# Kernel tuning notes

Measured on AMD Instinct MI355X. Metric: run time of the kernel, lower is better.

Reference implementation:

```python
import jax, jax.numpy as jnp
import numpy as np

N_NODES = 16   # number of per-node submodules in the DAG (topological order)
D = 2048       # per-node feature width (d_model)
B = 4096       # batch size of the in_graph tensor


def setup_inputs() -> dict:
    key = jax.random.key(0)
    kx, kw, kb = jax.random.split(key, 3)
    x = jax.random.normal(kx, (B, D), dtype=jnp.float32)
    # Per-node dense weights, scaled ~1/sqrt(D) so tanh stays in its linear-ish range
    W = jax.random.normal(kw, (N_NODES, D, D), dtype=jnp.float32) / np.float32(np.sqrt(D))
    b = jax.random.normal(kb, (N_NODES, D), dtype=jnp.float32) * np.float32(0.01)
    return {"x": x, "W": W, "b": b}


def reference(x, W, b):
    # Faithful DAG executor: iterate nodes in topological order; the address
    # book maps node i -> predecessor outputs {i-1, i-2} (node 0 reads x).
    # Each node module computes y = tanh(sum(inputs) @ W_i + b_i).
    # Loop is over the fixed structural node set (not a data dimension).
    outs = []
    for i in range(N_NODES):
        if i == 0:
            inp = x
        elif i == 1:
            inp = outs[0]
        else:
            inp = outs[i - 1] + outs[i - 2]  # address-book fan-in (sum of predecessors)
        y = jnp.tanh(inp @ W[i] + b[i])  # [B, D]
        outs.append(y)
    # _eval_forward returns the single terminal output of the DAG
    return outs[-1]
```

## Files before the change

### kernel.cpp

```cpp
#include <hip/hip_runtime.h>
#include <cstdint>
#include <cstddef>

#define NN 16
#define DD 2048
#define BB 4096

#define TM 256
#define TN 128
#define BK 64
#define BUFH (TM * BK + TN * BK)

typedef _Float16 half8 __attribute__((ext_vector_type(8)));
typedef _Float16 half4 __attribute__((ext_vector_type(4)));
typedef float f32x4 __attribute__((ext_vector_type(4)));

__device__ __forceinline__ float fast_tanh(float x) {
  float ax = __builtin_fabsf(x);
  float e = __expf(-2.0f * ax);
  float t = (1.0f - e) / (1.0f + e);
  return x < 0.0f ? -t : t;
}

__global__ __launch_bounds__(256) void wconv_kernel(const float* __restrict__ W,
                                                    _Float16* __restrict__ Wh) {
  __shared__ _Float16 tile[64][80];
  const int i = blockIdx.z;
  const int k0 = blockIdx.y * 64;
  const int n0 = blockIdx.x * 64;
  const float* Wi = W + (size_t)i * DD * DD;
  _Float16* Whi = Wh + (size_t)i * DD * DD;
  const int t = threadIdx.x;
  const int cr = t >> 4;
  const int cc = (t & 15) * 4;
#pragma unroll
  for (int p = 0; p < 4; ++p) {
    int r = p * 16 + cr;
    float4 v = *(const float4*)(Wi + (size_t)(k0 + r) * DD + n0 + cc);
    tile[cc + 0][r] = (_Float16)v.x;
    tile[cc + 1][r] = (_Float16)v.y;
    tile[cc + 2][r] = (_Float16)v.z;
    tile[cc + 3][r] = (_Float16)v.w;
  }
  __syncthreads();
  const int wr = t >> 3;
  const int wc = (t & 7) * 8;
#pragma unroll
  for (int p = 0; p < 2; ++p) {
    int n = p * 32 + wr;
    half8 v = *(const half8*)&tile[n][wc];
    *(half8*)(Whi + (size_t)(n0 + n) * DD + k0 + wc) = v;
  }
}

__global__ __launch_bounds__(256) void xconv_kernel(const float* __restrict__ x,
                                                    _Float16* __restrict__ s0) {
  size_t idx = (size_t)(blockIdx.x * 256 + threadIdx.x) * 4;
  float4 v = *(const float4*)(x + idx);
  half4 o;
  o.x = (_Float16)v.x; o.y = (_Float16)v.y; o.z = (_Float16)v.z; o.w = (_Float16)v.w;
  *(half4*)(s0 + idx) = o;
}

__global__ __launch_bounds__(512, 2) void node_gemm(
    const _Float16* __restrict__ S,
    const _Float16* __restrict__ Wt,
    const float* __restrict__ bias,
    _Float16* __restrict__ Y,
    const _Float16* __restrict__ Yprev,
    _Float16* __restrict__ Snext,
    float* __restrict__ Ofinal)
{
  __shared__ _Float16 smem[3 * BUFH];

  const int t = threadIdx.x;
  const int lane = t & 63;
  const int wave = t >> 6;
  const int bid = blockIdx.x;
  const int swz = (bid & 7) * 32 + (bid >> 3);
  const int n0 = (swz >> 4) * TN;
  const int m0 = (swz & 15) * TM;
  const int wm = (wave >> 1) * 64;
  const int wn = (wave & 1) * 64;
  const int lrow = lane & 15;
  const int lq = lane >> 4;

  f32x4 acc[4][4];
#pragma unroll
  for (int i = 0; i < 4; ++i)
#pragma unroll
    for (int j = 0; j < 4; ++j) acc[i][j] = (f32x4)0.0f;

  const int srow = t >> 3;
  const int ska = ((t & 7) ^ (srow & 7)) * 8;
  const _Float16* ag = S + (size_t)(m0 + srow) * DD + ska;
  const _Float16* bg = Wt + (size_t)(n0 + srow) * DD + ska;

  auto stage = [&](int buf, int k0) {
    const _Float16* a = ag + k0;
    const _Float16* b = bg + k0;
    _Float16* al = smem + buf * BUFH + t * 8;
    _Float16* bl = smem + buf * BUFH + TM * BK + t * 8;
#pragma unroll
    for (int r = 0; r < 4; ++r)
      __builtin_amdgcn_global_load_lds(
          (const __attribute__((address_space(1))) void*)(a + (size_t)(r * 64) * DD),
          (__attribute__((address_space(3))) void*)(al + r * 4096), 16, 0, 0);
#pragma unroll
    for (int r = 0; r < 2; ++r)
      __builtin_amdgcn_global_load_lds(
          (const __attribute__((address_space(1))) void*)(b + (size_t)(r * 64) * DD),
          (__attribute__((address_space(3))) void*)(bl + r * 4096), 16, 0, 0);
  };

  stage(0, 0);
  stage(1, BK);
  asm volatile("s_waitcnt vmcnt(6)" ::: "memory");
  asm volatile("s_barrier" ::: "memory");

  int cur = 0, nxt = 2;
  for (int i = 0; i < DD / BK; ++i) {
    if (i <= DD / BK - 3) stage(nxt, (i + 2) * BK);
    const _Float16* Ap = smem + cur * BUFH;
    const _Float16* Bp = smem + cur * BUFH + TM * BK;
#pragma unroll
    for (int ks = 0; ks < BK; ks += 32) {
      const int cx = (((ks >> 3) + lq) ^ (lrow & 7)) * 8;
      half8 a[4], b[4];
#pragma unroll
      for (int mt = 0; mt < 4; ++mt)
        a[mt] = *(const half8*)(Ap + (wm + mt * 16 + lrow) * BK + cx);
#pragma unroll
      for (int nt = 0; nt < 4; ++nt)
        b[nt] = *(const half8*)(Bp + (wn + nt * 16 + lrow) * BK + cx);
      __builtin_amdgcn_s_setprio(1);
#pragma unroll
      for (int mt = 0; mt < 4; ++mt)
#pragma unroll
        for (int nt = 0; nt < 4; ++nt)
          acc[mt][nt] =
              __builtin_amdgcn_mfma_f32_16x16x32_f16(a[mt], b[nt], acc[mt][nt], 0, 0, 0);
      __builtin_amdgcn_s_setprio(0);
    }
    if (i < DD / BK - 2) {
      asm volatile("s_waitcnt vmcnt(6)" ::: "memory");
      asm volatile("s_barrier" ::: "memory");
    } else if (i == DD / BK - 2) {
      asm volatile("s_waitcnt vmcnt(0)" ::: "memory");
      asm volatile("s_barrier" ::: "memory");
    }
    cur = (cur == 2) ? 0 : cur + 1;
    nxt = (nxt == 2) ? 0 : nxt + 1;
  }

  __syncthreads();
  _Float16* CT = smem;
  float bv[4];
#pragma unroll
  for (int nt = 0; nt < 4; ++nt) bv[nt] = bias[n0 + wn + nt * 16 + lrow];
#pragma unroll
  for (int mt = 0; mt < 4; ++mt)
#pragma unroll
    for (int nt = 0; nt < 4; ++nt)
#pragma unroll
      for (int r = 0; r < 4; ++r) {
        int row = wm + mt * 16 + lq * 4 + r;
        int col = wn + nt * 16 + lrow;
        CT[row * TN + col] = (_Float16)fast_tanh(acc[mt][nt][r] + bv[nt]);
      }
  __syncthreads();

#pragma unroll
  for (int pp = 0; pp < 8; ++pp) {
    int idx = pp * 4096 + t * 8;
    int row = idx >> 7;
    int col = idx & 127;
    size_t off = (size_t)(m0 + row) * DD + n0 + col;
    half8 y = *(const half8*)&CT[idx];
    if (Ofinal) {
      float4 f0 = {(float)y[0], (float)y[1], (float)y[2], (float)y[3]};
      float4 f1 = {(float)y[4], (float)y[5], (float)y[6], (float)y[7]};
      *(float4*)(Ofinal + off) = f0;
      *(float4*)(Ofinal + off + 4) = f1;
    } else {
      *(half8*)(Y + off) = y;
      half8 s = y;
      if (Yprev) s = s + *(const half8*)(Yprev + off);
      *(half8*)(Snext + off) = s;
    }
  }
}

extern "C" void kernel_launch(void* const* d_in, const int* in_sizes, int n_in,
                              void* d_out, int out_size, void* d_ws, size_t ws_size,
                              hipStream_t stream) {
  const float* x = (const float*)d_in[0];
  const float* W = (const float*)d_in[1];
  const float* b = (const float*)d_in[2];
  float* out = (float*)d_out;
  char* ws = (char*)d_ws;

  _Float16* Wh = (_Float16*)ws;
  size_t wbytes = (size_t)NN * DD * DD * sizeof(_Float16);
  _Float16* S0 = (_Float16*)(ws + wbytes);
  _Float16* S1 = S0 + (size_t)BB * DD;
  _Float16* Y0 = S1 + (size_t)BB * DD;
  _Float16* Y1 = Y0 + (size_t)BB * DD;

  wconv_kernel<<<dim3(DD / 64, DD / 64, NN), dim3(256), 0, stream>>>(W, Wh);
  xconv_kernel<<<dim3((BB * DD) / 1024), dim3(256), 0, stream>>>(x, S0);

  _Float16* Sb[2] = {S0, S1};
  _Float16* Yb[2] = {Y0, Y1};
  dim3 ggrid((BB / TM) * (DD / TN));
  for (int i = 0; i < NN; ++i) {
    const _Float16* Sin = Sb[i & 1];
    _Float16* Sout = Sb[(i + 1) & 1];
    _Float16* Yout = Yb[i & 1];
    const _Float16* Yp = (i >= 1) ? Yb[(i + 1) & 1] : nullptr;
    const bool last = (i == NN - 1);
    node_gemm<<<ggrid, dim3(512), 0, stream>>>(Sin, Wh + (size_t)i * DD * DD,
                                               b + (size_t)i * DD, Yout, Yp, Sout,
                                               last ? out : nullptr);
  }
  (void)in_sizes; (void)n_in; (void)out_size; (void)ws_size;
}
```

Before: 1.134 ms.

## Interleave prefetch issue with MFMA phases and remap tiles to XCD-local blocks

Splits each K-iteration into four phases. Each phase loads a subset of the A/B fragments from LDS, issues part of the next stage's global-to-LDS prefetch, hits a barrier, and runs eight MFMAs. This spreads memory issue across the compute instead of bursting it at loop start. The tile mapping is also changed so each XCD gets a contiguous 4x8 block of output tiles, which should improve L2 reuse of S rows and W columns. The extra barriers per iteration add synchronisation overhead and may stall waves.

```diff
diff --git a/kernel.cpp b/kernel.cpp
--- a/kernel.cpp
+++ b/kernel.cpp
@@ -77,9 +77,10 @@
   const int lane = t & 63;
   const int wave = t >> 6;
   const int bid = blockIdx.x;
-  const int swz = (bid & 7) * 32 + (bid >> 3);
-  const int n0 = (swz >> 4) * TN;
-  const int m0 = (swz & 15) * TM;
+  const int xcd = bid & 7;
+  const int loc = bid >> 3;
+  const int m0 = ((xcd & 3) * 4 + (loc & 3)) * TM;
+  const int n0 = ((xcd >> 2) * 8 + (loc >> 2)) * TN;
   const int wm = (wave >> 1) * 64;
   const int wn = (wave & 1) * 64;
   const int lrow = lane & 15;
@@ -96,16 +97,18 @@
   const _Float16* ag = S + (size_t)(m0 + srow) * DD + ska;
   const _Float16* bg = Wt + (size_t)(n0 + srow) * DD + ska;
 
-  auto stage = [&](int buf, int k0) {
+  auto stageA2 = [&](int buf, int k0, int r0) {
     const _Float16* a = ag + k0;
+    _Float16* al = smem + buf * BUFH + t * 8;
+#pragma unroll
+    for (int r = 0; r < 2; ++r)
+      __builtin_amdgcn_global_load_lds(
+          (const __attribute__((address_space(1))) void*)(a + (size_t)((r0 + r) * 64) * DD),
+          (__attribute__((address_space(3))) void*)(al + (r0 + r) * 4096), 16, 0, 0);
+  };
+  auto stageB2 = [&](int buf, int k0) {
     const _Float16* b = bg + k0;
-    _Float16* al = smem + buf * BUFH + t * 8;
     _Float16* bl = smem + buf * BUFH + TM * BK + t * 8;
-#pragma unroll
-    for (int r = 0; r < 4; ++r)
-      __builtin_amdgcn_global_load_lds(
-          (const __attribute__((address_space(1))) void*)(a + (size_t)(r * 64) * DD),
-          (__attribute__((address_space(3))) void*)(al + r * 4096), 16, 0, 0);
 #pragma unroll
     for (int r = 0; r < 2; ++r)
       __builtin_amdgcn_global_load_lds(
@@ -113,42 +116,79 @@
           (__attribute__((address_space(3))) void*)(bl + r * 4096), 16, 0, 0);
   };
 
-  stage(0, 0);
-  stage(1, BK);
+  stageA2(0, 0, 0); stageA2(0, 0, 2); stageB2(0, 0);
+  stageA2(1, BK, 0); stageA2(1, BK, 2); stageB2(1, BK);
   asm volatile("s_waitcnt vmcnt(6)" ::: "memory");
   asm volatile("s_barrier" ::: "memory");
 
   int cur = 0, nxt = 2;
   for (int i = 0; i < DD / BK; ++i) {
-    if (i <= DD / BK - 3) stage(nxt, (i + 2) * BK);
     const _Float16* Ap = smem + cur * BUFH;
     const _Float16* Bp = smem + cur * BUFH + TM * BK;
-#pragma unroll
-    for (int ks = 0; ks < BK; ks += 32) {
-      const int cx = (((ks >> 3) + lq) ^ (lrow & 7)) * 8;
-      half8 a[4], b[4];
-#pragma unroll
-      for (int mt = 0; mt < 4; ++mt)
-        a[mt] = *(const half8*)(Ap + (wm + mt * 16 + lrow) * BK + cx);
-#pragma unroll
-      for (int nt = 0; nt < 4; ++nt)
-        b[nt] = *(const half8*)(Bp + (wn + nt * 16 + lrow) * BK + cx);
-      __builtin_amdgcn_s_setprio(1);
-#pragma unroll
-      for (int mt = 0; mt < 4; ++mt)
-#pragma unroll
-        for (int nt = 0; nt < 4; ++nt)
-          acc[mt][nt] =
-              __builtin_amdgcn_mfma_f32_16x16x32_f16(a[mt], b[nt], acc[mt][nt], 0, 0, 0);
-      __builtin_amdgcn_s_setprio(0);
-    }
+    const bool pf = (i <= DD / BK - 3);
+    const int pk = (i + 2) * BK;
+    const int cx0 = ((0 + lq) ^ (lrow & 7)) * 8;
+    const int cx1 = ((4 + lq) ^ (lrow & 7)) * 8;
+    half8 a[4], b[4];
+
+#pragma unroll
+    for (int mt = 0; mt < 4; ++mt)
+      a[mt] = *(const half8*)(Ap + (wm + mt * 16 + lrow) * BK + cx0);
+    b[0] = *(const half8*)(Bp + (wn + 0 + lrow) * BK + cx0);
+    b[1] = *(const half8*)(Bp + (wn + 16 + lrow) * BK + cx0);
+    if (pf) stageA2(nxt, pk, 0);
+    asm volatile("s_barrier" ::: "memory");
+    __builtin_amdgcn_s_setprio(1);
+#pragma unroll
+    for (int mt = 0; mt < 4; ++mt) {
+      acc[mt][0] = __builtin_amdgcn_mfma_f32_16x16x32_f16(a[mt], b[0], acc[mt][0], 0, 0, 0);
+      acc[mt][1] = __builtin_amdgcn_mfma_f32_16x16x32_f16(a[mt], b[1], acc[mt][1], 0, 0, 0);
+    }
+    __builtin_amdgcn_s_setprio(0);
+
+    b[2] = *(const half8*)(Bp + (wn + 32 + lrow) * BK + cx0);
+    b[3] = *(const half8*)(Bp + (wn + 48 + lrow) * BK + cx0);
+    if (pf) stageA2(nxt, pk, 2);
+    asm volatile("s_barrier" ::: "memory");
+    __builtin_amdgcn_s_setprio(1);
+#pragma unroll
+    for (int mt = 0; mt < 4; ++mt) {
+      acc[mt][2] = __builtin_amdgcn_mfma_f32_16x16x32_f16(a[mt], b[2], acc[mt][2], 0, 0, 0);
+      acc[mt][3] = __builtin_amdgcn_mfma_f32_16x16x32_f16(a[mt], b[3], acc[mt][3], 0, 0, 0);
+    }
+    __builtin_amdgcn_s_setprio(0);
+
+#pragma unroll
+    for (int mt = 0; mt < 4; ++mt)
+      a[mt] = *(const half8*)(Ap + (wm + mt * 16 + lrow) * BK + cx1);
+    b[0] = *(const half8*)(Bp + (wn + 0 + lrow) * BK + cx1);
+    b[1] = *(const half8*)(Bp + (wn + 16 + lrow) * BK + cx1);
+    if (pf) stageB2(nxt, pk);
+    asm volatile("s_barrier" ::: "memory");
+    __builtin_amdgcn_s_setprio(1);
+#pragma unroll
+    for (int mt = 0; mt < 4; ++mt) {
+      acc[mt][0] = __builtin_amdgcn_mfma_f32_16x16x32_f16(a[mt], b[0], acc[mt][0], 0, 0, 0);
+      acc[mt][1] = __builtin_amdgcn_mfma_f32_16x16x32_f16(a[mt], b[1], acc[mt][1], 0, 0, 0);
+    }
+    __builtin_amdgcn_s_setprio(0);
+
+    b[2] = *(const half8*)(Bp + (wn + 32 + lrow) * BK + cx1);
+    b[3] = *(const half8*)(Bp + (wn + 48 + lrow) * BK + cx1);
     if (i < DD / BK - 2) {
       asm volatile("s_waitcnt vmcnt(6)" ::: "memory");
-      asm volatile("s_barrier" ::: "memory");
     } else if (i == DD / BK - 2) {
       asm volatile("s_waitcnt vmcnt(0)" ::: "memory");
-      asm volatile("s_barrier" ::: "memory");
-    }
+    }
+    asm volatile("s_barrier" ::: "memory");
+    __builtin_amdgcn_s_setprio(1);
+#pragma unroll
+    for (int mt = 0; mt < 4; ++mt) {
+      acc[mt][2] = __builtin_amdgcn_mfma_f32_16x16x32_f16(a[mt], b[2], acc[mt][2], 0, 0, 0);
+      acc[mt][3] = __builtin_amdgcn_mfma_f32_16x16x32_f16(a[mt], b[3], acc[mt][3], 0, 0, 0);
+    }
+    __builtin_amdgcn_s_setprio(0);
+
     cur = (cur == 2) ? 0 : cur + 1;
     nxt = (nxt == 2) ? 0 : nxt + 1;
   }
```

After: 1.113 ms. About the same (-1.9%).
